# Performance work log

Measured on AMD Instinct MI355X. Metric: run time of the kernel, lower is better.

Reference implementation:

```python
import jax, jax.numpy as jnp
import numpy as np

SUBSPACE_DIMS = np.array([1, 3, 3, 1])  # grade dims of 3D Clifford algebra (8 blades)
NUM_FEAT, NUM_HEADS, N_TOKENS, BS, C = 16, 8, 2048, 4, 8


def mv_linear(x, w, b):
    # x: [B, in, 8]; w: [out, in, 4] -> repeat over subspace dims -> [out, in, 8]
    wfull = jnp.repeat(w, SUBSPACE_DIMS, axis=-1)
    out = jnp.einsum('bic,oic->boc', x, wfull)
    return out.at[:, :, 0].add(b)  # bias on scalar blade only


def setup_inputs() -> dict:
    key = jax.random.key(0)
    ks = jax.random.split(key, 9)
    s = 0.05
    return {
        'feature_matrix': jax.random.normal(ks[0], (BS * N_TOKENS, NUM_FEAT, C), jnp.float32),
        'attention_mask': jnp.zeros((BS, N_TOKENS, N_TOKENS), jnp.float32),
        'wq': jax.random.normal(ks[1], (NUM_FEAT * NUM_HEADS, NUM_FEAT, 4), jnp.float32) * s,
        'bq': jax.random.normal(ks[2], (NUM_FEAT * NUM_HEADS,), jnp.float32) * s,
        'wk': jax.random.normal(ks[3], (NUM_FEAT * NUM_HEADS, NUM_FEAT, 4), jnp.float32) * s,
        'bk': jax.random.normal(ks[4], (NUM_FEAT * NUM_HEADS,), jnp.float32) * s,
        'wv': jax.random.normal(ks[5], (NUM_FEAT * NUM_HEADS, NUM_FEAT, 4), jnp.float32) * s,
        'bv': jax.random.normal(ks[6], (NUM_FEAT * NUM_HEADS,), jnp.float32) * s,
        'wo': jax.random.normal(ks[7], (NUM_FEAT, NUM_FEAT * NUM_HEADS, 4), jnp.float32) * s,
        'bo': jax.random.normal(ks[8], (NUM_FEAT,), jnp.float32) * s,
    }


def reference(feature_matrix, attention_mask, wq, bq, wk, bk, wv, bv, wo, bo):
    H, D = NUM_HEADS, NUM_FEAT
    n = N_TOKENS
    bs = feature_matrix.shape[0] // n

    def split_heads(t):  # [(bs n), (h d), c] -> [bs, h, n, d*c]
        return t.reshape(bs, n, H, D, C).transpose(0, 2, 1, 3, 4).reshape(bs, H, n, D * C)

    q = split_heads(mv_linear(feature_matrix, wq, bq)) / jnp.sqrt(jnp.float32(D * 8))
    k = split_heads(mv_linear(feature_matrix, wk, bk))
    v = split_heads(mv_linear(feature_matrix, wv, bv))

    attn = jnp.einsum('bhqe,bhke->bhqk', q, k) + attention_mask[:, None, :, :]
    attn = jax.nn.softmax(attn, axis=-1)
    out = jnp.einsum('bhqk,bhke->bhqe', attn, v)  # [bs, H, n, D*C]

    # transpose(1,2) then view(bs*n, H*D, 8)
    out = out.transpose(0, 2, 1, 3).reshape(bs * n, H * D, C)
    return mv_linear(out, wo, bo)
```

## Files before the change

### kernel.cpp

```cpp
#include <hip/hip_runtime.h>
#include <hip/hip_bf16.h>

typedef __attribute__((ext_vector_type(8))) __bf16 bf16x8;
typedef __attribute__((ext_vector_type(4))) float f32x4;
typedef __attribute__((ext_vector_type(8))) unsigned short ushort8;

#define TOKS 8192
#define LOG2E 1.4426950408889634f

__global__ __launch_bounds__(128) void proj_kernel(
    const float* __restrict__ x,
    const float* __restrict__ wq, const float* __restrict__ bq,
    const float* __restrict__ wk, const float* __restrict__ bk,
    const float* __restrict__ wv, const float* __restrict__ bv,
    __bf16* __restrict__ Qg, __bf16* __restrict__ Kg, __bf16* __restrict__ Vg)
{
    __shared__ float xs[512];
    const int tid = threadIdx.x;
    const int t0 = blockIdx.x * 4;
    ((float4*)xs)[tid] = ((const float4*)(x + (size_t)t0 * 128))[tid];
    __syncthreads();
    const int o = tid, h = o >> 4, d = o & 15;

    float acc[3][4][8];
#pragma unroll
    for (int tz = 0; tz < 3; ++tz) {
        const float bias = (tz == 0 ? bq : tz == 1 ? bk : bv)[o];
#pragma unroll
        for (int t = 0; t < 4; ++t) {
            acc[tz][t][0] = bias;
#pragma unroll
            for (int c = 1; c < 8; ++c) acc[tz][t][c] = 0.f;
        }
    }
    const float4* w40 = (const float4*)(wq + o * 64);
    const float4* w41 = (const float4*)(wk + o * 64);
    const float4* w42 = (const float4*)(wv + o * 64);
    for (int i = 0; i < 16; ++i) {
        float4 wv3[3] = {w40[i], w41[i], w42[i]};
#pragma unroll
        for (int t = 0; t < 4; ++t) {
            f32x4 xlo = *(const f32x4*)(xs + t * 128 + i * 8);
            f32x4 xhi = *(const f32x4*)(xs + t * 128 + i * 8 + 4);
            float xv[8] = {xlo[0], xlo[1], xlo[2], xlo[3],
                           xhi[0], xhi[1], xhi[2], xhi[3]};
#pragma unroll
            for (int tz = 0; tz < 3; ++tz) {
                float wr[8] = {wv3[tz].x, wv3[tz].y, wv3[tz].y, wv3[tz].y,
                               wv3[tz].z, wv3[tz].z, wv3[tz].z, wv3[tz].w};
#pragma unroll
                for (int c = 0; c < 8; ++c) acc[tz][t][c] += xv[c] * wr[c];
            }
        }
    }
    const int bb = t0 >> 11, tt0 = t0 & 2047;
    size_t base = (((size_t)(bb * 8 + h)) * 2048 + tt0) * 128 + d * 8;
#pragma unroll
    for (int tz = 0; tz < 3; ++tz) {
        __bf16* Og = tz == 0 ? Qg : tz == 1 ? Kg : Vg;
        const float scale = (tz == 0) ? (0.08838834764831845f * LOG2E) : 1.0f;
#pragma unroll
        for (int t = 0; t < 4; ++t) {
            bf16x8 v;
#pragma unroll
            for (int c = 0; c < 8; ++c) v[c] = (__bf16)(acc[tz][t][c] * scale);
            *(bf16x8*)(Og + base + (size_t)t * 128) = v;
        }
    }
}

__global__ __launch_bounds__(256) void transv_kernel(
    const __bf16* __restrict__ Vg, __bf16* __restrict__ Vt)
{
    __shared__ __align__(16) char T[16384];
    const int tid = threadIdx.x;
    const int bh = blockIdx.y, t0 = blockIdx.x * 64;
    const __bf16* src = Vg + ((size_t)bh * 2048 + t0) * 128;
#pragma unroll
    for (int it = 0; it < 4; ++it) {
        int cidx = it * 256 + tid;
        int r = cidx >> 4, e0 = (cidx & 15) * 8;
        bf16x8 v = *(const bf16x8*)(src + r * 128 + e0);
        *(bf16x8*)(T + ((r * 256 + e0 * 2) ^ ((r & 7) << 4))) = v;
    }
    __syncthreads();
    const int e = tid & 127, half = tid >> 7;
    __bf16* dst = Vt + ((size_t)bh * 128 + e) * 2048 + t0 + half * 32;
#pragma unroll
    for (int jc = 0; jc < 4; ++jc) {
        ushort8 o8;
#pragma unroll
        for (int j = 0; j < 8; ++j) {
            int t = half * 32 + jc * 8 + j;
            o8[j] = *(const unsigned short*)(T + ((t * 256 + e * 2) ^ ((t & 7) << 4)));
        }
        *(ushort8*)(dst + jc * 8) = o8;
    }
}

__global__ __launch_bounds__(256) void flash_kernel(
    const __bf16* __restrict__ Qg, const __bf16* __restrict__ Kg,
    const __bf16* __restrict__ Vtg, const float* __restrict__ mask,
    __bf16* __restrict__ AO)
{
    __shared__ __align__(16) char Kl[16384];
    __shared__ __align__(16) char Vl[16384];

    const int tid = threadIdx.x;
    const int lane = tid & 63, w = tid >> 6;
    const int l15 = lane & 15, lg = lane >> 4;

    const int wid = blockIdx.y * 32 + blockIdx.x;
    const int xcd = wid & 7, j = wid >> 3;
    const int bh = (xcd << 2) | (j & 3);
    const int q0 = (j >> 2) * 64;
    const int b = bh >> 3;

    int kg[4], klb[4], vg[4], vlb[4];
#pragma unroll
    for (int it = 0; it < 4; ++it) {
        int cidx = it * 256 + tid;
        int kv = cidx >> 4, c15 = cidx & 15;
        int skv = (kv & 3) | (((kv >> 3) & 1) << 2);
        kg[it] = kv * 128 + c15 * 8;
        klb[it] = kv * 256 + ((c15 ^ skv) * 16);
        int e = cidx >> 3, jj = cidx & 7;
        vg[it] = e * 2048 + jj * 8;
        vlb[it] = e * 128 + ((jj * 16) ^ ((e & 7) << 4));
    }
    const __bf16* kbase = Kg + (size_t)bh * 2048 * 128;
    const __bf16* vtbase = Vtg + (size_t)bh * 128 * 2048;
    const float* mbase = mask + ((size_t)b * 2048 + q0 + w * 16 + l15) * 2048;

    bf16x8 qf[4];
    {
        const __bf16* qp = Qg + ((size_t)bh * 2048 + q0 + w * 16 + l15) * 128 + lg * 8;
#pragma unroll
        for (int ks = 0; ks < 4; ++ks) qf[ks] = *(const bf16x8*)(qp + ks * 32);
    }

    f32x4 o_acc[8];
#pragma unroll
    for (int i = 0; i < 8; ++i) o_acc[i] = (f32x4){0.f, 0.f, 0.f, 0.f};
    f32x4 lacc4 = (f32x4){0.f, 0.f, 0.f, 0.f};

    const int ksw = (l15 & 7) << 4;
    const int kb15 = (((l15 >> 2) << 3) + (l15 & 3)) * 256;
    const char* krd0 = Kl + kb15 + ((lg * 16) ^ ksw);
    const char* krd1 = Kl + kb15 + ((64 + lg * 16) ^ ksw);
    const char* krd2 = Kl + kb15 + ((128 + lg * 16) ^ ksw);
    const char* krd3 = Kl + kb15 + ((192 + lg * 16) ^ ksw);
    const char* vrd0 = Vl + l15 * 128 + ((lg * 16) ^ ksw);
    const char* vrd1 = Vl + l15 * 128 + ((64 + lg * 16) ^ ksw);

    bf16x8 kreg[4], vreg[4];
#pragma unroll
    for (int it = 0; it < 4; ++it) {
        kreg[it] = *(const bf16x8*)(kbase + kg[it]);
        vreg[it] = *(const bf16x8*)(vtbase + vg[it]);
    }
#pragma unroll
    for (int it = 0; it < 4; ++it) {
        *(bf16x8*)(Kl + klb[it]) = kreg[it];
        *(bf16x8*)(Vl + vlb[it]) = vreg[it];
    }
    const __bf16* kpt = kbase;
    const __bf16* vpt = vtbase;
    const float* mp = mbase + lg * 8;
    f32x4 mr[4];
#pragma unroll
    for (int ct = 0; ct < 4; ++ct) {
        f32x4 mv = *(const f32x4*)(mp + (ct & 1) * 32 + ((ct >> 1) << 2));
#pragma unroll
        for (int r = 0; r < 4; ++r) mr[ct][r] = mv[r] * LOG2E;
    }

    for (int kv0 = 0; kv0 < 2048; kv0 += 64) {
        __syncthreads();
        const bool more = (kv0 + 64) < 2048;
        if (more) {
            kpt += 8192;
            vpt += 64;
#pragma unroll
            for (int it = 0; it < 4; ++it) {
                kreg[it] = *(const bf16x8*)(kpt + kg[it]);
                vreg[it] = *(const bf16x8*)(vpt + vg[it]);
            }
        }

        f32x4 st[4];
        __builtin_amdgcn_s_setprio(1);
#pragma unroll
        for (int ct = 0; ct < 4; ++ct) {
            const int co = (ct & 1) * 8192 + (ct >> 1) * 1024;
            f32x4 acc = mr[ct];
            acc = __builtin_amdgcn_mfma_f32_16x16x32_bf16(*(const bf16x8*)(krd0 + co), qf[0], acc, 0, 0, 0);
            acc = __builtin_amdgcn_mfma_f32_16x16x32_bf16(*(const bf16x8*)(krd1 + co), qf[1], acc, 0, 0, 0);
            acc = __builtin_amdgcn_mfma_f32_16x16x32_bf16(*(const bf16x8*)(krd2 + co), qf[2], acc, 0, 0, 0);
            acc = __builtin_amdgcn_mfma_f32_16x16x32_bf16(*(const bf16x8*)(krd3 + co), qf[3], acc, 0, 0, 0);
            st[ct] = acc;
        }
        __builtin_amdgcn_s_setprio(0);

        union { __bf16 h[8]; bf16x8 v; } pk0, pk1;
#pragma unroll
        for (int ct = 0; ct < 4; ct += 2) {
#pragma unroll
            for (int r = 0; r < 4; ++r) {
                float p = exp2f(st[ct][r]);
                lacc4[r] += p;
                pk0.h[((ct >> 1) << 2) + r] = (__bf16)p;
            }
        }
        __builtin_amdgcn_s_setprio(1);
#pragma unroll
        for (int ct2 = 0; ct2 < 8; ++ct2)
            o_acc[ct2] = __builtin_amdgcn_mfma_f32_16x16x32_bf16(
                *(const bf16x8*)(vrd0 + ct2 * 2048), pk0.v, o_acc[ct2], 0, 0, 0);
        __builtin_amdgcn_s_setprio(0);
#pragma unroll
        for (int ct = 1; ct < 4; ct += 2) {
#pragma unroll
            for (int r = 0; r < 4; ++r) {
                float p = exp2f(st[ct][r]);
                lacc4[r] += p;
                pk1.h[((ct >> 1) << 2) + r] = (__bf16)p;
            }
        }
        __builtin_amdgcn_s_setprio(1);
#pragma unroll
        for (int ct2 = 0; ct2 < 8; ++ct2)
            o_acc[ct2] = __builtin_amdgcn_mfma_f32_16x16x32_bf16(
                *(const bf16x8*)(vrd1 + ct2 * 2048), pk1.v, o_acc[ct2], 0, 0, 0);
        __builtin_amdgcn_s_setprio(0);
        __syncthreads();

        if (more) {
#pragma unroll
            for (int it = 0; it < 4; ++it) {
                *(bf16x8*)(Kl + klb[it]) = kreg[it];
                *(bf16x8*)(Vl + vlb[it]) = vreg[it];
            }
            mp += 64;
#pragma unroll
            for (int ct = 0; ct < 4; ++ct) {
                f32x4 mv = *(const f32x4*)(mp + (ct & 1) * 32 + ((ct >> 1) << 2));
#pragma unroll
                for (int r = 0; r < 4; ++r) mr[ct][r] = mv[r] * LOG2E;
            }
        }
    }

    float tot = (lacc4[0] + lacc4[1]) + (lacc4[2] + lacc4[3]);
    tot += __shfl_xor(tot, 16);
    tot += __shfl_xor(tot, 32);
    const float linv = 1.0f / tot;
    const size_t tok = (size_t)b * 2048 + q0 + w * 16 + l15;
    __bf16* aop = AO + tok * 1024 + (bh & 7) * 128;
#pragma unroll
    for (int ct2 = 0; ct2 < 8; ++ct2) {
        union { __bf16 h[4]; unsigned long long u64; } ov;
#pragma unroll
        for (int r = 0; r < 4; ++r) ov.h[r] = (__bf16)(o_acc[ct2][r] * linv);
        *(unsigned long long*)(aop + ct2 * 16 + lg * 4) = ov.u64;
    }
}

__global__ __launch_bounds__(128) void outproj_kernel(
    const __bf16* __restrict__ AO, const float* __restrict__ wo,
    const float* __restrict__ bo, float* __restrict__ out)
{
    __shared__ float al[8 * 1032];
    const int tid = threadIdx.x;
    const int t0 = blockIdx.x * 8;
#pragma unroll
    for (int it = 0; it < 8; ++it) {
        bf16x8 v = *(const bf16x8*)(AO + (size_t)(t0 + it) * 1024 + tid * 8);
        f32x4 lo = {(float)v[0], (float)v[1], (float)v[2], (float)v[3]};
        f32x4 hi = {(float)v[4], (float)v[5], (float)v[6], (float)v[7]};
        *(f32x4*)(al + it * 1032 + tid * 8) = lo;
        *(f32x4*)(al + it * 1032 + tid * 8 + 4) = hi;
    }
    __syncthreads();
    const int o = tid >> 3, t = tid & 7;
    float acc[8];
    acc[0] = bo[o];
#pragma unroll
    for (int c = 1; c < 8; ++c) acc[c] = 0.f;
    const float4* w4 = (const float4*)wo + o * 128;
    for (int ii = 0; ii < 128; ++ii) {
        float4 wv = w4[ii];
        f32x4 xlo = *(const f32x4*)(al + t * 1032 + ii * 8);
        f32x4 xhi = *(const f32x4*)(al + t * 1032 + ii * 8 + 4);
        float wr[8] = {wv.x, wv.y, wv.y, wv.y, wv.z, wv.z, wv.z, wv.w};
        float xv[8] = {xlo[0], xlo[1], xlo[2], xlo[3], xhi[0], xhi[1], xhi[2], xhi[3]};
#pragma unroll
        for (int c = 0; c < 8; ++c) acc[c] += xv[c] * wr[c];
    }
    float* op = out + (size_t)(t0 + t) * 128 + o * 8;
    *(float4*)op = (float4){acc[0], acc[1], acc[2], acc[3]};
    *(float4*)(op + 4) = (float4){acc[4], acc[5], acc[6], acc[7]};
}

extern "C" void kernel_launch(void* const* d_in, const int* in_sizes, int n_in,
                              void* d_out, int out_size, void* d_ws, size_t ws_size,
                              hipStream_t stream)
{
    const float* x    = (const float*)d_in[0];
    const float* mask = (const float*)d_in[1];
    const float* wq   = (const float*)d_in[2];
    const float* bq   = (const float*)d_in[3];
    const float* wk   = (const float*)d_in[4];
    const float* bk   = (const float*)d_in[5];
    const float* wv   = (const float*)d_in[6];
    const float* bv   = (const float*)d_in[7];
    const float* wo   = (const float*)d_in[8];
    const float* bo   = (const float*)d_in[9];
    float* out = (float*)d_out;

    const size_t SLOT = (size_t)32 * 2048 * 128;
    const size_t need = SLOT * 4 * 2;
    if (ws_size < need) {
        hipMemsetAsync(d_out, 0, (size_t)out_size * sizeof(float), stream);
        return;
    }
    __bf16* Qg = (__bf16*)d_ws;
    __bf16* Kg = Qg + SLOT;
    __bf16* Vg = Kg + SLOT;
    __bf16* Vt = Vg + SLOT;
    __bf16* AO = Vg;

    proj_kernel<<<TOKS / 4, 128, 0, stream>>>(x, wq, bq, wk, bk, wv, bv, Qg, Kg, Vg);
    transv_kernel<<<dim3(32, 32), 256, 0, stream>>>(Vg, Vt);
    flash_kernel<<<dim3(32, 32), 256, 0, stream>>>(Qg, Kg, Vt, mask, AO);
    outproj_kernel<<<TOKS / 8, 128, 0, stream>>>(AO, wo, bo, out);
}
```

Baseline: 188.7 us.

## Use direct global-to-LDS loads with double-buffered K/V in flash kernel

The flash attention kernel now fetches K and V tiles with global_load_lds straight into shared memory, instead of staging them through registers. The swizzle moves from the LDS write address to the global read address. K and V are double-buffered, so the next tile's load and the mask prefetch overlap the current tile's MFMA work, and one __syncthreads per iteration is dropped. In exchange, LDS use per block doubles to 64KB, which may cut the number of resident blocks per CU.

```diff
diff --git a/kernel.cpp b/kernel.cpp
--- a/kernel.cpp
+++ b/kernel.cpp
@@ -7,6 +7,12 @@
 
 #define TOKS 8192
 #define LOG2E 1.4426950408889634f
+
+__device__ inline void gld16(const __bf16* g, void* l) {
+    __builtin_amdgcn_global_load_lds(
+        (const __attribute__((address_space(1))) unsigned int*)g,
+        (__attribute__((address_space(3))) unsigned int*)l, 16, 0, 0);
+}
 
 __global__ __launch_bounds__(128) void proj_kernel(
     const float* __restrict__ x,
@@ -103,8 +109,7 @@
     const __bf16* __restrict__ Vtg, const float* __restrict__ mask,
     __bf16* __restrict__ AO)
 {
-    __shared__ __align__(16) char Kl[16384];
-    __shared__ __align__(16) char Vl[16384];
+    __shared__ __align__(16) char Slab[65536];
 
     const int tid = threadIdx.x;
     const int lane = tid & 63, w = tid >> 6;
@@ -116,21 +121,20 @@
     const int q0 = (j >> 2) * 64;
     const int b = bh >> 3;
 
-    int kg[4], klb[4], vg[4], vlb[4];
+    int kgo[4], vgo[4];
 #pragma unroll
     for (int it = 0; it < 4; ++it) {
         int cidx = it * 256 + tid;
         int kv = cidx >> 4, c15 = cidx & 15;
         int skv = (kv & 3) | (((kv >> 3) & 1) << 2);
-        kg[it] = kv * 128 + c15 * 8;
-        klb[it] = kv * 256 + ((c15 ^ skv) * 16);
+        kgo[it] = kv * 128 + ((c15 ^ skv) * 8);
         int e = cidx >> 3, jj = cidx & 7;
-        vg[it] = e * 2048 + jj * 8;
-        vlb[it] = e * 128 + ((jj * 16) ^ ((e & 7) << 4));
-    }
+        vgo[it] = e * 2048 + ((jj ^ (e & 7)) * 8);
+    }
+    const int ldsb = w * 1024;
     const __bf16* kbase = Kg + (size_t)bh * 2048 * 128;
     const __bf16* vtbase = Vtg + (size_t)bh * 128 * 2048;
-    const float* mbase = mask + ((size_t)b * 2048 + q0 + w * 16 + l15) * 2048;
+    const float* mp = mask + ((size_t)b * 2048 + q0 + w * 16 + l15) * 2048 + lg * 8;
 
     bf16x8 qf[4];
     {
@@ -146,28 +150,19 @@
 
     const int ksw = (l15 & 7) << 4;
     const int kb15 = (((l15 >> 2) << 3) + (l15 & 3)) * 256;
-    const char* krd0 = Kl + kb15 + ((lg * 16) ^ ksw);
-    const char* krd1 = Kl + kb15 + ((64 + lg * 16) ^ ksw);
-    const char* krd2 = Kl + kb15 + ((128 + lg * 16) ^ ksw);
-    const char* krd3 = Kl + kb15 + ((192 + lg * 16) ^ ksw);
-    const char* vrd0 = Vl + l15 * 128 + ((lg * 16) ^ ksw);
-    const char* vrd1 = Vl + l15 * 128 + ((64 + lg * 16) ^ ksw);
-
-    bf16x8 kreg[4], vreg[4];
+    const int kinv0 = kb15 + ((lg * 16) ^ ksw);
+    const int kinv1 = kb15 + ((64 + lg * 16) ^ ksw);
+    const int kinv2 = kb15 + ((128 + lg * 16) ^ ksw);
+    const int kinv3 = kb15 + ((192 + lg * 16) ^ ksw);
+    const int vinv0 = l15 * 128 + ((lg * 16) ^ ksw);
+    const int vinv1 = l15 * 128 + ((64 + lg * 16) ^ ksw);
+
 #pragma unroll
     for (int it = 0; it < 4; ++it) {
-        kreg[it] = *(const bf16x8*)(kbase + kg[it]);
-        vreg[it] = *(const bf16x8*)(vtbase + vg[it]);
-    }
-#pragma unroll
-    for (int it = 0; it < 4; ++it) {
-        *(bf16x8*)(Kl + klb[it]) = kreg[it];
-        *(bf16x8*)(Vl + vlb[it]) = vreg[it];
-    }
-    const __bf16* kpt = kbase;
-    const __bf16* vpt = vtbase;
-    const float* mp = mbase + lg * 8;
-    f32x4 mr[4];
+        gld16(kbase + kgo[it], Slab + it * 4096 + ldsb);
+        gld16(vtbase + vgo[it], Slab + 32768 + it * 4096 + ldsb);
+    }
+    f32x4 mr[4], mrN[4];
 #pragma unroll
     for (int ct = 0; ct < 4; ++ct) {
         f32x4 mv = *(const f32x4*)(mp + (ct & 1) * 32 + ((ct >> 1) << 2));
@@ -175,18 +170,33 @@
         for (int r = 0; r < 4; ++r) mr[ct][r] = mv[r] * LOG2E;
     }
 
+    int cur = 0;
     for (int kv0 = 0; kv0 < 2048; kv0 += 64) {
         __syncthreads();
         const bool more = (kv0 + 64) < 2048;
+
         if (more) {
-            kpt += 8192;
-            vpt += 64;
+            const __bf16* kp = kbase + (size_t)(kv0 + 64) * 128;
+            const __bf16* vp = vtbase + (kv0 + 64);
+            char* kd = Slab + (cur ^ 1) * 16384 + ldsb;
+            char* vd = Slab + 32768 + (cur ^ 1) * 16384 + ldsb;
 #pragma unroll
             for (int it = 0; it < 4; ++it) {
-                kreg[it] = *(const bf16x8*)(kpt + kg[it]);
-                vreg[it] = *(const bf16x8*)(vpt + vg[it]);
-            }
-        }
+                gld16(kp + kgo[it], kd + it * 4096);
+                gld16(vp + vgo[it], vd + it * 4096);
+            }
+            const float* mpn = mp + kv0 + 64;
+#pragma unroll
+            for (int ct = 0; ct < 4; ++ct) {
+                f32x4 mv = *(const f32x4*)(mpn + (ct & 1) * 32 + ((ct >> 1) << 2));
+#pragma unroll
+                for (int r = 0; r < 4; ++r) mrN[ct][r] = mv[r] * LOG2E;
+            }
+        }
+        __builtin_amdgcn_sched_barrier(0);
+
+        const char* kl = Slab + cur * 16384;
+        const char* vl = Slab + 32768 + cur * 16384;
 
         f32x4 st[4];
         __builtin_amdgcn_s_setprio(1);
@@ -194,10 +204,10 @@
         for (int ct = 0; ct < 4; ++ct) {
             const int co = (ct & 1) * 8192 + (ct >> 1) * 1024;
             f32x4 acc = mr[ct];
-            acc = __builtin_amdgcn_mfma_f32_16x16x32_bf16(*(const bf16x8*)(krd0 + co), qf[0], acc, 0, 0, 0);
-            acc = __builtin_amdgcn_mfma_f32_16x16x32_bf16(*(const bf16x8*)(krd1 + co), qf[1], acc, 0, 0, 0);
-            acc = __builtin_amdgcn_mfma_f32_16x16x32_bf16(*(const bf16x8*)(krd2 + co), qf[2], acc, 0, 0, 0);
-            acc = __builtin_amdgcn_mfma_f32_16x16x32_bf16(*(const bf16x8*)(krd3 + co), qf[3], acc, 0, 0, 0);
+            acc = __builtin_amdgcn_mfma_f32_16x16x32_bf16(*(const bf16x8*)(kl + kinv0 + co), qf[0], acc, 0, 0, 0);
+            acc = __builtin_amdgcn_mfma_f32_16x16x32_bf16(*(const bf16x8*)(kl + kinv1 + co), qf[1], acc, 0, 0, 0);
+            acc = __builtin_amdgcn_mfma_f32_16x16x32_bf16(*(const bf16x8*)(kl + kinv2 + co), qf[2], acc, 0, 0, 0);
+            acc = __builtin_amdgcn_mfma_f32_16x16x32_bf16(*(const bf16x8*)(kl + kinv3 + co), qf[3], acc, 0, 0, 0);
             st[ct] = acc;
         }
         __builtin_amdgcn_s_setprio(0);
@@ -216,7 +226,7 @@
 #pragma unroll
         for (int ct2 = 0; ct2 < 8; ++ct2)
             o_acc[ct2] = __builtin_amdgcn_mfma_f32_16x16x32_bf16(
-                *(const bf16x8*)(vrd0 + ct2 * 2048), pk0.v, o_acc[ct2], 0, 0, 0);
+                *(const bf16x8*)(vl + vinv0 + ct2 * 2048), pk0.v, o_acc[ct2], 0, 0, 0);
         __builtin_amdgcn_s_setprio(0);
 #pragma unroll
         for (int ct = 1; ct < 4; ct += 2) {
@@ -231,24 +241,14 @@
 #pragma unroll
         for (int ct2 = 0; ct2 < 8; ++ct2)
             o_acc[ct2] = __builtin_amdgcn_mfma_f32_16x16x32_bf16(
-                *(const bf16x8*)(vrd1 + ct2 * 2048), pk1.v, o_acc[ct2], 0, 0, 0);
+                *(const bf16x8*)(vl + vinv1 + ct2 * 2048), pk1.v, o_acc[ct2], 0, 0, 0);
         __builtin_amdgcn_s_setprio(0);
-        __syncthreads();
 
         if (more) {
 #pragma unroll
-            for (int it = 0; it < 4; ++it) {
-                *(bf16x8*)(Kl + klb[it]) = kreg[it];
-                *(bf16x8*)(Vl + vlb[it]) = vreg[it];
-            }
-            mp += 64;
-#pragma unroll
-            for (int ct = 0; ct < 4; ++ct) {
-                f32x4 mv = *(const f32x4*)(mp + (ct & 1) * 32 + ((ct >> 1) << 2));
-#pragma unroll
-                for (int r = 0; r < 4; ++r) mr[ct][r] = mv[r] * LOG2E;
-            }
-        }
+            for (int ct = 0; ct < 4; ++ct) mr[ct] = mrN[ct];
+        }
+        cur ^= 1;
     }
 
     float tot = (lacc4[0] + lacc4[1]) + (lacc4[2] + lacc4[3]);
```

Result: slower. 207.0 us (+9.7%).
